# Kernel optimization log

Hardware: AMD Instinct MI355X
Metric: run time of the kernel (lower is better)

## Reference

```python
import jax, jax.numpy as jnp
import numpy as np

PH, PW = 7, 7  # pooled_height, pooled_width
B, H, W, C, R = 4, 64, 64, 256, 128


def setup_inputs() -> dict:
    key = jax.random.key(0)
    k1, k2, k3 = jax.random.split(key, 3)
    feature_map = jax.random.normal(k1, (B, H, W, C), dtype=jnp.float32)
    # ROIs: (y_min, x_min, y_max, x_max) relative coords; sized so every
    # region has >= PH rows / PW cols (avoids empty-bin -inf edge case).
    start = jax.random.uniform(k2, (B, R, 2), minval=0.0, maxval=0.4)
    extent = jax.random.uniform(k3, (B, R, 2), minval=0.3, maxval=0.55)
    rois = jnp.concatenate([start, start + extent], axis=-1).astype(jnp.float32)
    return {"feature_map": feature_map, "rois": rois}


def _pool_image(fm, rois_img):
    # fm: (H, W, C); rois_img: (R, 4)
    h, w, _ = fm.shape
    # tf.cast(float->int32) truncates; coords are non-negative so == floor
    h0 = jnp.floor(h * rois_img[:, 0]).astype(jnp.int32)
    w0 = jnp.floor(w * rois_img[:, 1]).astype(jnp.int32)
    h1 = jnp.floor(h * rois_img[:, 2]).astype(jnp.int32)
    w1 = jnp.floor(w * rois_img[:, 3]).astype(jnp.int32)
    rh, rw = h1 - h0, w1 - w0
    hstep = jnp.maximum(rh // PH, 1)  # guard: assumes region >= pooled grid
    wstep = jnp.maximum(rw // PW, 1)

    # Map each absolute row/col to its pooled bin (or PH/PW = "outside").
    rel_h = jnp.arange(h)[None, :] - h0[:, None]            # (R, H)
    bin_h = jnp.clip(rel_h // hstep[:, None], 0, PH - 1)     # last bin extends to region end
    row_id = jnp.where((rel_h >= 0) & (rel_h < rh[:, None]), bin_h, PH)
    rel_w = jnp.arange(w)[None, :] - w0[:, None]            # (R, W)
    bin_w = jnp.clip(rel_w // wstep[:, None], 0, PW - 1)
    col_id = jnp.where((rel_w >= 0) & (rel_w < rw[:, None]), bin_w, PW)

    # Stage 1: segment-max over rows -> (R, PH, W, C)
    seg_rows = jax.vmap(
        lambda ids: jax.ops.segment_max(fm, ids, num_segments=PH + 1)
    )(row_id)[:, :PH]

    # Stage 2: segment-max over cols -> (R, PH, PW, C)
    def col_pool(t, ids):  # t: (PH, W, C)
        tt = jnp.swapaxes(t, 0, 1)  # (W, PH, C)
        s = jax.ops.segment_max(tt, ids, num_segments=PW + 1)[:PW]
        return jnp.swapaxes(s, 0, 1)  # (PH, PW, C)

    return jax.vmap(col_pool)(seg_rows, col_id)


def reference(feature_map, rois):
    # (B, R, PH, PW, C)
    return jax.vmap(_pool_image)(feature_map, rois)
```

## Files before the change

kernel.cpp:

```cpp
#include <hip/hip_runtime.h>
#include <math.h>

#define PH 7
#define PW 7
#define BB 4
#define HH 64
#define WW 64
#define CC 256
#define RR 128
#define CH4 (CC / 4)
#define BINS_PER_IMG (RR * PH * PW)
#define NBINS (BB * BINS_PER_IMG)
#define NBLK (NBINS / 4)
#define BLK_PER_IMG (NBLK / 8)

typedef float f4 __attribute__((ext_vector_type(4)));

__device__ __forceinline__ f4 max4(f4 a, f4 b) {
    f4 r;
    r.x = fmaxf(a.x, b.x); r.y = fmaxf(a.y, b.y);
    r.z = fmaxf(a.z, b.z); r.w = fmaxf(a.w, b.w);
    return r;
}

__global__ __launch_bounds__(256) void ROIPoolingLayer_62079457296467_kernel(
    const float* __restrict__ fm, const float* __restrict__ rois,
    float* __restrict__ out)
{
    const int wave = threadIdx.x >> 6;
    const int lane = threadIdx.x & 63;

    const int bid   = blockIdx.x;
    const int xcd   = bid & 7;
    const int slot  = bid >> 3;
    const int b     = xcd >> 1;
    const int blkin = (xcd & 1) * BLK_PER_IMG + slot;
    const int local = blkin * 4 + wave;
    const int r     = local / (PH * PW);
    const int bin   = local - r * (PH * PW);
    const int ph    = bin / PW;
    const int pw    = bin - ph * PW;
    const int br    = b * RR + r;

    const f4 roi = ((const f4*)rois)[br];
    const int h0 = (int)floorf((float)HH * roi.x);
    const int w0 = (int)floorf((float)WW * roi.y);
    const int h1 = (int)floorf((float)HH * roi.z);
    const int w1 = (int)floorf((float)WW * roi.w);
    const int rh = h1 - h0;
    const int rw = w1 - w0;
    const int hstep = max(rh / PH, 1);
    const int wstep = max(rw / PW, 1);

    int hs = h0 + ph * hstep;
    int he = (ph == PH - 1) ? (h0 + rh) : (hs + hstep);
    he = min(he, h0 + rh);  he = min(he, HH);
    int ws = w0 + pw * wstep;
    int we = (pw == PW - 1) ? (w0 + rw) : (ws + wstep);
    we = min(we, w0 + rw);  we = min(we, WW);

    const int hbin = he - hs;
    const int wbin = we - ws;
    const int npix = hbin * wbin;

    const f4* __restrict__ fmb =
        (const f4*)fm + ((size_t)b * HH + hs) * (WW * CH4) + (size_t)ws * CH4 + lane;

    f4 acc = (f4){-INFINITY, -INFINITY, -INFINITY, -INFINITY};

    if (npix > 0) {
        const unsigned m = (65536u + (unsigned)wbin - 1) / (unsigned)wbin;
        for (int p = 0; p < npix; p += 8) {
            f4 v[8];
#pragma unroll
            for (int k = 0; k < 8; ++k) {
                const int pk = min(p + k, npix - 1);
                const int q  = (int)(((unsigned)pk * m) >> 16);
                const int w  = pk - q * wbin;
                v[k] = fmb[((size_t)q * WW + w) * CH4];
            }
#pragma unroll
            for (int k = 0; k < 8; ++k)
                acc = max4(acc, v[k]);
        }
    }

    const size_t gbin = (size_t)b * BINS_PER_IMG + local;
    __builtin_nontemporal_store(acc, (f4*)out + gbin * CH4 + lane);
}

extern "C" void kernel_launch(void* const* d_in, const int* in_sizes, int n_in,
                              void* d_out, int out_size, void* d_ws, size_t ws_size,
                              hipStream_t stream) {
    const float* fm   = (const float*)d_in[0];
    const float* rois = (const float*)d_in[1];
    float* out        = (float*)d_out;
    ROIPoolingLayer_62079457296467_kernel<<<NBLK, 256, 0, stream>>>(fm, rois, out);
}
```

Before: 88.50 us.

## Precompute 2x2 max pyramid tables and pool bins from downsampled levels

Adds a pre-pass kernel that builds 2x2 pooled, row-pair and column-pair max tables in workspace. The main kernel then covers each bin's interior with the 2x2 table, its odd edges with the row or column tables, and its corners with raw pixels, so each bin does roughly four times fewer loads. In exchange there is an extra kernel launch and the tables are written and read back from memory, about double the feature map's size. It also relies on the workspace being large enough.

```diff
diff --git a/kernel.cpp b/kernel.cpp
--- a/kernel.cpp
+++ b/kernel.cpp
@@ -14,6 +14,10 @@
 #define NBLK (NBINS / 4)
 #define BLK_PER_IMG (NBLK / 8)
 
+#define P2_OFF 0
+#define C2_OFF (BB * 32 * 32 * CH4)
+#define R2_OFF (C2_OFF + BB * 32 * 64 * CH4)
+
 typedef float f4 __attribute__((ext_vector_type(4)));
 
 __device__ __forceinline__ f4 max4(f4 a, f4 b) {
@@ -23,9 +27,44 @@
     return r;
 }
 
+
+__global__ __launch_bounds__(256) void roi_build_pyr(
+    const float* __restrict__ fm, float* __restrict__ tab)
+{
+    const int wave = threadIdx.x >> 6;
+    const int lane = threadIdx.x & 63;
+    const int bid  = blockIdx.x;
+    const int xcd  = bid & 7;
+    const int slot = bid >> 3;
+    const int b    = xcd >> 1;
+    const int ci   = (xcd & 1) * 512 + slot * 4 + wave;
+    const int h2   = ci >> 5;
+    const int w2   = ci & 31;
+
+    const f4* fp = (const f4*)fm + ((size_t)(b * HH + 2 * h2) * WW + 2 * w2) * CH4 + lane;
+    const f4 v00 = fp[0];
+    const f4 v01 = fp[CH4];
+    const f4 v10 = fp[WW * CH4];
+    const f4 v11 = fp[WW * CH4 + CH4];
+    const f4 r0 = max4(v00, v01);
+    const f4 r1 = max4(v10, v11);
+    const f4 c0 = max4(v00, v10);
+    const f4 c1 = max4(v01, v11);
+    const f4 p  = max4(r0, r1);
+
+    f4* P2 = (f4*)tab + P2_OFF;
+    f4* C2 = (f4*)tab + C2_OFF;
+    f4* R2 = (f4*)tab + R2_OFF;
+    P2[((b * 32 + h2) * 32 + w2) * CH4 + lane]          = p;
+    C2[((b * 32 + h2) * 64 + 2 * w2) * CH4 + lane]      = c0;
+    C2[((b * 32 + h2) * 64 + 2 * w2 + 1) * CH4 + lane]  = c1;
+    R2[((b * 64 + 2 * h2) * 32 + w2) * CH4 + lane]      = r0;
+    R2[((b * 64 + 2 * h2 + 1) * 32 + w2) * CH4 + lane]  = r1;
+}
+
 __global__ __launch_bounds__(256) void ROIPoolingLayer_62079457296467_kernel(
     const float* __restrict__ fm, const float* __restrict__ rois,
-    float* __restrict__ out)
+    const float* __restrict__ tab, float* __restrict__ out)
 {
     const int wave = threadIdx.x >> 6;
     const int lane = threadIdx.x & 63;
@@ -55,35 +94,63 @@
     int hs = h0 + ph * hstep;
     int he = (ph == PH - 1) ? (h0 + rh) : (hs + hstep);
     he = min(he, h0 + rh);  he = min(he, HH);
-    int ws = w0 + pw * wstep;
-    int we = (pw == PW - 1) ? (w0 + rw) : (ws + wstep);
-    we = min(we, w0 + rw);  we = min(we, WW);
+    int cs = w0 + pw * wstep;
+    int ce = (pw == PW - 1) ? (w0 + rw) : (cs + wstep);
+    ce = min(ce, w0 + rw);  ce = min(ce, WW);
 
-    const int hbin = he - hs;
-    const int wbin = we - ws;
-    const int npix = hbin * wbin;
+    const int h2a = (hs + 1) >> 1, h2b = he >> 1;
+    const int w2a = (cs + 1) >> 1, w2b = ce >> 1;
+    const int hA = h2b - h2a, wA = w2b - w2a;
+    const int ft = hs & 1, fb = he & 1;
+    const int fl = cs & 1, fr = ce & 1;
 
-    const f4* __restrict__ fmb =
-        (const f4*)fm + ((size_t)b * HH + hs) * (WW * CH4) + (size_t)ws * CH4 + lane;
+    const f4* P2 = (const f4*)tab + P2_OFF;
+    const f4* C2 = (const f4*)tab + C2_OFF;
+    const f4* R2 = (const f4*)tab + R2_OFF;
 
     f4 acc = (f4){-INFINITY, -INFINITY, -INFINITY, -INFINITY};
 
-    if (npix > 0) {
-        const unsigned m = (65536u + (unsigned)wbin - 1) / (unsigned)wbin;
-        for (int p = 0; p < npix; p += 8) {
-            f4 v[8];
+    const int nA = hA * wA;
+    if (nA > 0) {
+        const unsigned m = (65536u + (unsigned)wA - 1) / (unsigned)wA;
+        const f4* bp = P2 + ((size_t)(b * 32 + h2a) * 32 + w2a) * CH4 + lane;
+        for (int p = 0; p < nA; p += 4) {
+            f4 v[4];
 #pragma unroll
-            for (int k = 0; k < 8; ++k) {
-                const int pk = min(p + k, npix - 1);
+            for (int k = 0; k < 4; ++k) {
+                const int pk = min(p + k, nA - 1);
                 const int q  = (int)(((unsigned)pk * m) >> 16);
-                const int w  = pk - q * wbin;
-                v[k] = fmb[((size_t)q * WW + w) * CH4];
+                const int w  = pk - q * wA;
+                v[k] = bp[(q * 32 + w) * CH4];
             }
 #pragma unroll
-            for (int k = 0; k < 8; ++k)
-                acc = max4(acc, v[k]);
+            for (int k = 0; k < 4; ++k) acc = max4(acc, v[k]);
         }
     }
+
+    if (ft) {
+        const f4* rp = R2 + ((size_t)(b * 64 + hs) * 32 + w2a) * CH4 + lane;
+        for (int i = 0; i < wA; ++i) acc = max4(acc, rp[i * CH4]);
+    }
+    if (fb) {
+        const f4* rp = R2 + ((size_t)(b * 64 + (he - 1)) * 32 + w2a) * CH4 + lane;
+        for (int i = 0; i < wA; ++i) acc = max4(acc, rp[i * CH4]);
+    }
+
+    if (fl) {
+        const f4* cp = C2 + ((size_t)(b * 32 + h2a) * 64 + cs) * CH4 + lane;
+        for (int i = 0; i < hA; ++i) acc = max4(acc, cp[(size_t)i * 64 * CH4]);
+    }
+    if (fr) {
+        const f4* cp = C2 + ((size_t)(b * 32 + h2a) * 64 + (ce - 1)) * CH4 + lane;
+        for (int i = 0; i < hA; ++i) acc = max4(acc, cp[(size_t)i * 64 * CH4]);
+    }
+
+    const f4* fb4 = (const f4*)fm + (size_t)b * HH * WW * CH4 + lane;
+    if (ft & fl) acc = max4(acc, fb4[(hs * WW + cs) * CH4]);
+    if (ft & fr) acc = max4(acc, fb4[(hs * WW + (ce - 1)) * CH4]);
+    if (fb & fl) acc = max4(acc, fb4[((he - 1) * WW + cs) * CH4]);
+    if (fb & fr) acc = max4(acc, fb4[((he - 1) * WW + (ce - 1)) * CH4]);
 
     const size_t gbin = (size_t)b * BINS_PER_IMG + local;
     __builtin_nontemporal_store(acc, (f4*)out + gbin * CH4 + lane);
@@ -95,5 +162,7 @@
     const float* fm   = (const float*)d_in[0];
     const float* rois = (const float*)d_in[1];
     float* out        = (float*)d_out;
-    ROIPoolingLayer_62079457296467_kernel<<<NBLK, 256, 0, stream>>>(fm, rois, out);
+    float* tab        = (float*)d_ws;
+    roi_build_pyr<<<1024, 256, 0, stream>>>(fm, tab);
+    ROIPoolingLayer_62079457296467_kernel<<<NBLK, 256, 0, stream>>>(fm, rois, tab, out);
 }
```

New measurement: 88.45 us. About the same (-0.1%).
